# Optimization experiments

Measured on AMD Instinct MI355X. Metric: run time of the kernel, lower is better.

## Reference

```python
import jax, jax.numpy as jnp
import numpy as np

FRAME = 160      # frame_size
K = 15           # frames_per_payload
ORDER = 12       # lpc_order
B = 4096
T = K * FRAME    # 2400


def setup_inputs() -> dict:
    key = jax.random.key(0)
    k1, k2 = jax.random.split(key)
    bits = jax.random.randint(k1, (B, K), 0, 2, dtype=jnp.int32)
    pcm = jax.random.uniform(k2, (B, T, 1), jnp.float32, minval=-1.0, maxval=1.0)
    alpha = jnp.float32(0.05)  # layer weight 'alpha' (alpha_init=0.05)
    return {"bits": bits, "pcm": pcm, "alpha": alpha}


def lpc_burg(x, order):
    """librosa.lpc (Burg's method), vectorized over all frames. x: (N, L)."""
    a = jnp.zeros((x.shape[0], order + 1), x.dtype).at[:, 0].set(1.0)
    f = x[:, 1:]          # forward prediction error
    b = x[:, :-1]         # backward prediction error
    den = jnp.sum(f * f + b * b, axis=-1)
    for i in range(order):  # small fixed-order unrolled loop
        reflect = -2.0 * jnp.sum(b * f, axis=-1) / den   # (N,)
        r = reflect[:, None]
        # a[j] <- a[j] + reflect * a[i+1-j] for j=0..i+1 (j=0 is a no-op since a[i+1]=0)
        a = a.at[:, : i + 2].set(a[:, : i + 2] + r * a[:, : i + 2][:, ::-1])
        f_tmp = f
        f = f + r * b
        b = b + r * f_tmp
        den = (1.0 - reflect * reflect) * den - b[:, -1] ** 2 - f[:, 0] ** 2
        f = f[:, 1:]
        b = b[:, :-1]
    return a  # (N, order+1), a[:,0]==1


def fir_filter(a, x):
    """scipy.signal.lfilter(a, [1.0], x): out[n] = sum_k a[k]*x[n-k], zero init."""
    L = x.shape[1]
    xpad = jnp.pad(x, ((0, 0), (ORDER, 0)))
    # X[:, n, k] = x[:, n-k]
    X = jnp.stack([xpad[:, ORDER - k: ORDER - k + L] for k in range(ORDER + 1)], axis=-1)
    return jnp.einsum('nlk,nk->nl', X, a)


def residual(pcm):
    # pcm: (B, T, 1) -> per-frame LPC residual, same shape
    frames = pcm[..., 0].reshape(-1, FRAME)                 # (B*K, FRAME)
    win = jnp.asarray(np.hanning(FRAME), dtype=pcm.dtype)   # Hann window for LPC analysis only
    a = lpc_burg(frames * win, ORDER)
    res = fir_filter(a, frames)                              # filter the RAW frame
    return res.reshape(pcm.shape[0], T, 1)


def reference(bits, pcm, alpha):
    res = residual(pcm)
    signs = 2.0 * bits.astype(pcm.dtype) - 1.0              # (B, K) in {-1,+1}
    chips = jnp.repeat(signs, FRAME, axis=1)[..., None]     # (B, T, 1)
    return pcm + alpha * res * chips
```

## Files before the change

### kernel.cpp

```cpp
#include <hip/hip_runtime.h>

#define FRAME 160
#define KFR 15
#define ORDER 12
#define NFRAMES (4096 * KFR)
#define EPL 10
#define FPW 4

__device__ __forceinline__ float gred16(float v) {
#pragma unroll
    for (int m = 1; m < 16; m <<= 1) v += __shfl_xor(v, m, 64);
    return v;
}

__global__ __launch_bounds__(256) void ResidualEmbedding_70798240907390_kernel(
    const int* __restrict__ bits, const float* __restrict__ pcm,
    const float* __restrict__ alpha_p, float* __restrict__ out)
{
    const int wave = threadIdx.x >> 6;
    const int lane = threadIdx.x & 63;
    const int g    = lane >> 4;
    const int s    = lane & 15;
    const int wf0  = (blockIdx.x * 4 + wave) * FPW;
    const int f_id = wf0 + g;

    __shared__ float s_frame[4][FPW][FRAME];

    {
        const float4* src = (const float4*)(pcm + (size_t)wf0 * FRAME);
        float4* dst = (float4*)&s_frame[wave][0][0];
        dst[lane]      = src[lane];
        dst[lane + 64] = src[lane + 64];
        if (lane < 32) dst[lane + 128] = src[lane + 128];
    }
    __syncthreads();
    const float* xf = &s_frame[wave][g][0];

    const int p0 = s * EPL;
    const float w2p = 6.2831853071795864769f / 159.0f;

    float F[EPL], B[EPL];
    float dpart = 0.0f;
    float wprev = 0.5f - 0.5f * __cosf(w2p * (float)p0);
#pragma unroll
    for (int t = 0; t < EPL; ++t) {
        int p = p0 + t;
        float wnext = 0.5f - 0.5f * __cosf(w2p * (float)(p + 1));
        if (p < FRAME - 1) {
            float b0 = xf[p] * wprev;
            float f0 = xf[p + 1] * wnext;
            F[t] = f0; B[t] = b0;
            dpart += f0 * f0 + b0 * b0;
        } else { F[t] = 0.0f; B[t] = 0.0f; }
        wprev = wnext;
    }
    float den = gred16(dpart);

    float a = (s == 0) ? 1.0f : 0.0f;

#pragma unroll
    for (int i = 0; i < ORDER; ++i) {
        float p = 0.0f;
#pragma unroll
        for (int t = 0; t < EPL; ++t) p = fmaf(F[t], B[t], p);
        float num = gred16(p);
        float r = -2.0f * num / den;

        int rs = i + 1 - s;
        float arev = __shfl(a, g * 16 + (rs < 0 ? 0 : rs), 64);
        if (s <= i + 1) a = fmaf(r, arev, a);

        float nF[EPL], nB[EPL];
#pragma unroll
        for (int t = 0; t < EPL; ++t) {
            nF[t] = fmaf(r, B[t], F[t]);
            nB[t] = fmaf(r, F[t], B[t]);
        }

        const int pe = 158 - i;
        const int SL = pe / EPL, SS = pe % EPL;
        float blast  = __shfl(nB[SS], g * 16 + SL, 64);
        float ffirst = __shfl(nF[0], g * 16, 64);
        den = (1.0f - r * r) * den - blast * blast - ffirst * ffirst;

        float up = __shfl_down(nF[0], 1, 16);
#pragma unroll
        for (int t = 0; t < EPL - 1; ++t) F[t] = nF[t + 1];
        F[EPL - 1] = (s == 15) ? 0.0f : up;
#pragma unroll
        for (int t = 0; t < EPL; ++t) B[t] = nB[t];
        if (s == SL) B[SS] = 0.0f;
    }

    float ak[ORDER + 1];
#pragma unroll
    for (int k = 0; k <= ORDER; ++k) ak[k] = __shfl(a, g * 16 + k, 64);

    float xr[EPL + ORDER];
#pragma unroll
    for (int j = 0; j < EPL + ORDER; ++j) {
        int m = p0 - ORDER + j;
        xr[j] = (m >= 0) ? xf[m] : 0.0f;
    }

    const float ac = alpha_p[0] * (2.0f * (float)bits[f_id] - 1.0f);
    float res[EPL];
#pragma unroll
    for (int t = 0; t < EPL; ++t) {
        float acc = 0.0f;
#pragma unroll
        for (int k = 0; k <= ORDER; ++k)
            acc = fmaf(ak[k], xr[ORDER + t - k], acc);
        res[t] = fmaf(ac, acc, xr[ORDER + t]);
    }
    float2* og = (float2*)(out + (size_t)f_id * FRAME + p0);
#pragma unroll
    for (int t = 0; t < EPL / 2; ++t)
        og[t] = make_float2(res[2 * t], res[2 * t + 1]);
}

extern "C" void kernel_launch(void* const* d_in, const int* in_sizes, int n_in,
                              void* d_out, int out_size, void* d_ws, size_t ws_size,
                              hipStream_t stream) {
    const int*   bits  = (const int*)d_in[0];
    const float* pcm   = (const float*)d_in[1];
    const float* alpha = (const float*)d_in[2];
    float*       out   = (float*)d_out;

    dim3 grid(NFRAMES / 16), block(256);
    hipLaunchKernelGGL(ResidualEmbedding_70798240907390_kernel, grid, block, 0, stream,
                       bits, pcm, alpha, out);
}
```

Measured before the change: 110.5 us.

## Replace wave shuffles with DPP row reductions and restructure Burg recurrence

Swaps the ds_bpermute-based xor shuffles for DPP row operations (quad_perm, row_shr) in the 16-lane reductions and shifts. The LPC coefficient update now keeps a mirrored copy in each lane, shifted by a DPP row shift, which removes the indexed shuffle. The denominator update is split so its edge terms are folded into the next iteration's reduction, and the divide becomes a hardware reciprocal. Coefficients are gathered through LDS instead of shuffles. The rcp approximation may slightly change numerics, and the reversed-coefficient trick relies on zeroed lanes behaving correctly at row boundaries.

```diff
diff --git a/kernel.cpp b/kernel.cpp
--- a/kernel.cpp
+++ b/kernel.cpp
@@ -1,15 +1,22 @@
 #include <hip/hip_runtime.h>
 
 #define FRAME 160
-#define KFR 15
 #define ORDER 12
-#define NFRAMES (4096 * KFR)
+#define NFRAMES (4096 * 15)
 #define EPL 10
 #define FPW 4
 
-__device__ __forceinline__ float gred16(float v) {
-#pragma unroll
-    for (int m = 1; m < 16; m <<= 1) v += __shfl_xor(v, m, 64);
+template<int CTRL>
+__device__ __forceinline__ float dppf(float v) {
+    return __int_as_float(__builtin_amdgcn_update_dpp(
+        0, __float_as_int(v), CTRL, 0xF, 0xF, true));
+}
+
+__device__ __forceinline__ float rowsum16(float v) {
+    v += dppf<0xB1>(v);
+    v += dppf<0x4E>(v);
+    v += dppf<0x140>(v);
+    v += dppf<0x141>(v);
     return v;
 }
 
@@ -25,6 +32,7 @@
     const int f_id = wf0 + g;
 
     __shared__ float s_frame[4][FPW][FRAME];
+    __shared__ float s_a[4][FPW][16];
 
     {
         const float4* src = (const float4*)(pcm + (size_t)wf0 * FRAME);
@@ -40,7 +48,7 @@
     const float w2p = 6.2831853071795864769f / 159.0f;
 
     float F[EPL], B[EPL];
-    float dpart = 0.0f;
+    float dp0 = 0.0f, dp1 = 0.0f;
     float wprev = 0.5f - 0.5f * __cosf(w2p * (float)p0);
 #pragma unroll
     for (int t = 0; t < EPL; ++t) {
@@ -50,25 +58,34 @@
             float b0 = xf[p] * wprev;
             float f0 = xf[p + 1] * wnext;
             F[t] = f0; B[t] = b0;
-            dpart += f0 * f0 + b0 * b0;
+            dp0 = fmaf(f0, f0, dp0);
+            dp1 = fmaf(b0, b0, dp1);
         } else { F[t] = 0.0f; B[t] = 0.0f; }
         wprev = wnext;
     }
-    float den = gred16(dpart);
+    float den = rowsum16(dp0 + dp1);
 
-    float a = (s == 0) ? 1.0f : 0.0f;
+    float a  = (s == 0) ? 1.0f : 0.0f;
+    float ar = (s == 1) ? 1.0f : 0.0f;
+    float cpart = 0.0f;
+    float denScaled = 0.0f;
 
 #pragma unroll
     for (int i = 0; i < ORDER; ++i) {
-        float p = 0.0f;
+        float q0 = 0.0f, q1 = 0.0f;
 #pragma unroll
-        for (int t = 0; t < EPL; ++t) p = fmaf(F[t], B[t], p);
-        float num = gred16(p);
-        float r = -2.0f * num / den;
+        for (int t = 0; t < EPL; t += 2) {
+            q0 = fmaf(F[t],     B[t],     q0);
+            q1 = fmaf(F[t + 1], B[t + 1], q1);
+        }
+        float num = rowsum16(q0 + q1);
+        if (i > 0) den = denScaled - rowsum16(cpart);
+        float r = -2.0f * num * __builtin_amdgcn_rcpf(den);
 
-        int rs = i + 1 - s;
-        float arev = __shfl(a, g * 16 + (rs < 0 ? 0 : rs), 64);
-        if (s <= i + 1) a = fmaf(r, arev, a);
+        float a_new  = fmaf(r, ar, a);
+        float ar_new = fmaf(r, a, ar);
+        a  = a_new;
+        ar = dppf<0x111>(ar_new);
 
         float nF[EPL], nB[EPL];
 #pragma unroll
@@ -79,22 +96,25 @@
 
         const int pe = 158 - i;
         const int SL = pe / EPL, SS = pe % EPL;
-        float blast  = __shfl(nB[SS], g * 16 + SL, 64);
-        float ffirst = __shfl(nF[0], g * 16, 64);
-        den = (1.0f - r * r) * den - blast * blast - ffirst * ffirst;
+        float fe = (s == 0)  ? nF[0]  : 0.0f;
+        float be = (s == SL) ? nB[SS] : 0.0f;
+        cpart = fmaf(fe, fe, be * be);
+        denScaled = fmaf(-r * r, den, den);
 
-        float up = __shfl_down(nF[0], 1, 16);
+        float up = dppf<0x101>(nF[0]);
 #pragma unroll
         for (int t = 0; t < EPL - 1; ++t) F[t] = nF[t + 1];
-        F[EPL - 1] = (s == 15) ? 0.0f : up;
+        F[EPL - 1] = up;
 #pragma unroll
         for (int t = 0; t < EPL; ++t) B[t] = nB[t];
-        if (s == SL) B[SS] = 0.0f;
+        B[SS] = (s == SL) ? 0.0f : B[SS];
     }
 
+    s_a[wave][g][s] = a;
+    __syncthreads();
     float ak[ORDER + 1];
 #pragma unroll
-    for (int k = 0; k <= ORDER; ++k) ak[k] = __shfl(a, g * 16 + k, 64);
+    for (int k = 0; k <= ORDER; ++k) ak[k] = s_a[wave][g][k];
 
     float xr[EPL + ORDER];
 #pragma unroll
```

Measured after the change: 111.4 us. Within noise of the previous version (+0.9%).
